# Optimization experiments

Hardware: AMD Instinct MI355X
Metric: run time of the kernel (lower is better)

The kernel has to match this reference:

```python
import jax, jax.numpy as jnp
import numpy as np

B, N, D = 512, 256, 16   # batch, tokens (num_patches+1), embed_dim (= n_qubits)
STAGES = 4               # log2(D) butterfly stages


def _safe_acos(u):
    # matches torch acos + nan_to_num: out-of-range -> 0, with clean gradients
    ok = jnp.abs(u) <= 1.0
    return jnp.where(ok, jnp.arccos(jnp.clip(u, -1.0, 1.0)), 0.0)


def get_rbs_parameters(x):
    # x: [B, N, D] -> RBS angles [B, N, D-1]; recursive spherical-coordinate decomposition
    a0 = _safe_acos(x[..., 0])
    def step(carry, xi):
        t, a_prev = carry
        inv = jnp.nan_to_num(1.0 / jnp.sin(a_prev))
        t = t * inv
        a = _safe_acos(xi * t)
        return (t, a), a
    xs = jnp.moveaxis(x[..., 1:D - 1], -1, 0)  # [D-2, B, N]
    _, rest = jax.lax.scan(step, (jnp.ones_like(a0), a0), xs)
    alphas = jnp.concatenate([a0[None], rest], axis=0)  # [D-1, B, N]
    return jnp.moveaxis(alphas, 0, -1)


def amplitudes(alphas):
    # unary-state amplitudes prepared by the diagonal vector loader
    # a_i = cos(alpha_i) * prod_{k<i} sin(alpha_k);  a_{D-1} = prod_k sin(alpha_k)
    sins = jnp.sin(alphas)
    prefix = jnp.concatenate([jnp.ones_like(sins[..., :1]), jnp.cumprod(sins, axis=-1)], axis=-1)  # [B,N,D]
    return jnp.concatenate([prefix[..., :D - 1] * jnp.cos(alphas), prefix[..., D - 1:]], axis=-1)


def butterfly_matrix(angles):
    # orthogonal DxD matrix implemented by the Butterfly RBS circuit in the unary subspace
    d = 2 * angles.shape[1]
    M = jnp.eye(d, dtype=angles.dtype)
    for s in range(angles.shape[0]):
        step = 1 << s
        idx_i = np.array([i for i in range(d) if (i // step) % 2 == 0])
        idx_j = idx_i + step
        c = jnp.cos(angles[s])[:, None]
        sn = jnp.sin(angles[s])[:, None]
        Mi, Mj = M[idx_i], M[idx_j]
        M = M.at[idx_i].set(c * Mi + sn * Mj)
        M = M.at[idx_j].set(-sn * Mi + c * Mj)
    return M


def layer_norm(x, g, b, eps=1e-5):
    mu = jnp.mean(x, -1, keepdims=True)
    var = jnp.var(x, -1, keepdims=True)
    return (x - mu) / jnp.sqrt(var + eps) * g + b


def setup_inputs() -> dict:
    key = jax.random.key(0)
    ks = jax.random.split(key, 4)
    return {
        "x": jax.random.normal(ks[0], (B, N, D), jnp.float32),
        "ln1_g": jnp.ones((D,), jnp.float32),
        "ln1_b": jnp.zeros((D,), jnp.float32),
        "angles": jax.random.normal(ks[1], (STAGES, D // 2), jnp.float32),
        "ln2_g": jnp.ones((D,), jnp.float32),
        "ln2_b": jnp.zeros((D,), jnp.float32),
        "w1": jax.random.normal(ks[2], (D, 4 * D), jnp.float32) / np.sqrt(D).astype(np.float32),
        "b1": jnp.zeros((4 * D,), jnp.float32),
        "w2": jax.random.normal(ks[3], (4 * D, D), jnp.float32) / np.sqrt(4 * D).astype(np.float32),
        "b2": jnp.zeros((D,), jnp.float32),
    }


def reference(x, ln1_g, ln1_b, angles, ln2_g, ln2_b, w1, b1, w2, b2):
    inp = layer_norm(x, ln1_g, ln1_b) / 2.0
    alphas = jnp.nan_to_num(get_rbs_parameters(inp))
    a = amplitudes(alphas)                 # [B,N,D] loaded unary amplitudes
    W = butterfly_matrix(angles)           # [D,D] orthogonal butterfly
    Wa = jnp.einsum('de,bne->bnd', W, a)   # [B,N,D]
    vxT = jnp.abs(Wa)
    # xwx[b,i,j] = sqrt(P(qubit0=1)) = |<a_j| W |a_i>| for the xWx circuit
    xwx = jnp.abs(jnp.einsum('bid,bjd->bij', Wa, a))
    attn = jax.nn.softmax(xwx, axis=-1)
    x = x + jnp.einsum('bij,bjd->bid', attn, vxT)
    h = layer_norm(x, ln2_g, ln2_b)
    h = jax.nn.gelu(h @ w1 + b1, approximate=False) @ w2 + b2
    return x + h
```

## Files before the change

kernel.cpp:

```cpp
#include <hip/hip_runtime.h>
#include <math.h>

#define NTOK 256
#define DD 16
#define BDIM 256

typedef short short8 __attribute__((ext_vector_type(8)));
typedef float f32x16 __attribute__((ext_vector_type(16)));
typedef unsigned int u32;
typedef unsigned long long u64;

__device__ __forceinline__ u32 f2bf(float f) {
    u32 u = __float_as_uint(f);
    u += 0x7FFFu + ((u >> 16) & 1u);
    return u >> 16;
}
struct U128 { u64 a, b; };
__device__ __forceinline__ short8 ld8(const unsigned short* p) {
    U128 t;
    t.a = *(const u64*)(p);
    t.b = *(const u64*)(p + 4);
    return __builtin_bit_cast(short8, t);
}
__device__ __forceinline__ void pack_swap16(f32x16 p, short8& f0, short8& f1) {
    u32 W00, W01, W10, W11, W20, W21, W30, W31;
    asm("v_cvt_pk_bf16_f32 %0, %1, %2" : "=v"(W00) : "v"(p[0]),  "v"(p[1]));
    asm("v_cvt_pk_bf16_f32 %0, %1, %2" : "=v"(W01) : "v"(p[2]),  "v"(p[3]));
    asm("v_cvt_pk_bf16_f32 %0, %1, %2" : "=v"(W10) : "v"(p[4]),  "v"(p[5]));
    asm("v_cvt_pk_bf16_f32 %0, %1, %2" : "=v"(W11) : "v"(p[6]),  "v"(p[7]));
    asm("v_cvt_pk_bf16_f32 %0, %1, %2" : "=v"(W20) : "v"(p[8]),  "v"(p[9]));
    asm("v_cvt_pk_bf16_f32 %0, %1, %2" : "=v"(W21) : "v"(p[10]), "v"(p[11]));
    asm("v_cvt_pk_bf16_f32 %0, %1, %2" : "=v"(W30) : "v"(p[12]), "v"(p[13]));
    asm("v_cvt_pk_bf16_f32 %0, %1, %2" : "=v"(W31) : "v"(p[14]), "v"(p[15]));
    asm("v_permlane32_swap_b32 %0, %1" : "+v"(W00), "+v"(W10));
    asm("v_permlane32_swap_b32 %0, %1" : "+v"(W01), "+v"(W11));
    asm("v_permlane32_swap_b32 %0, %1" : "+v"(W20), "+v"(W30));
    asm("v_permlane32_swap_b32 %0, %1" : "+v"(W21), "+v"(W31));
    struct { u32 x, y, z, w; } i0{W00, W01, W10, W11}, i1{W20, W21, W30, W31};
    f0 = __builtin_bit_cast(short8, i0);
    f1 = __builtin_bit_cast(short8, i1);
}
__device__ __forceinline__ float gelu_erf(float v) {
    float xx = v * 0.70710678118654752f;
    float ax = fabsf(xx);
    float t = __builtin_amdgcn_rcpf(__builtin_fmaf(0.3275911f, ax, 1.0f));
    float poly = t * (0.254829592f + t * (-0.284496736f + t * (1.421413741f
               + t * (-1.453152027f + t * 1.061405429f))));
    float r = 1.0f - poly * __expf(-ax * ax);
    float e = copysignf(r, xx);
    return 0.5f * v * (1.0f + e);
}

__global__ __launch_bounds__(BDIM, 4) void qab_kernel(
    const float* __restrict__ x,
    const float* __restrict__ ln1_g, const float* __restrict__ ln1_b,
    const float* __restrict__ angles,
    const float* __restrict__ ln2_g, const float* __restrict__ ln2_b,
    const float* __restrict__ w1, const float* __restrict__ b1,
    const float* __restrict__ w2, const float* __restrict__ b2,
    float* __restrict__ out)
{
    __shared__ alignas(16) unsigned short a_bf[NTOK][20];
    __shared__ alignas(16) unsigned short wa_bf[NTOK][20];
    __shared__ alignas(16) unsigned short vxT[17][268];
    __shared__ alignas(16) unsigned short w1tb[64][20];
    __shared__ alignas(16) unsigned short w2tb[16][68];
    __shared__ alignas(16) float b1_lds[64];
    __shared__ alignas(16) float ln2g_lds[DD];
    __shared__ alignas(16) float ln2b_lds[DD];
    __shared__ alignas(16) float b2_lds[DD];

    const int b     = blockIdx.x >> 1;
    const int half  = blockIdx.x & 1;
    const int tid   = threadIdx.x;
    const int r     = tid;
    const int wv    = tid >> 6;
    const int strip = half * 4 + wv;
    const int l31   = tid & 31;
    const int hi    = (tid >> 5) & 1;
    const int lane  = tid & 63;

    const float* xres = x + ((size_t)b * NTOK + 32 * strip + l31) * DD;
    const float4 xra = *(const float4*)(xres + 4 * hi);
    const float4 xrb = *(const float4*)(xres + 8 + 4 * hi);

    f32x16 zc;
    #pragma unroll
    for (int t = 0; t < 16; ++t) zc[t] = 0.0f;

    float amp[DD];
    {
        const float* xrow = x + ((size_t)b * NTOK + r) * DD;
        float xr[DD];
        #pragma unroll
        for (int qq = 0; qq < 4; ++qq) {
            float4 v = ((const float4*)xrow)[qq];
            xr[4*qq+0] = v.x; xr[4*qq+1] = v.y; xr[4*qq+2] = v.z; xr[4*qq+3] = v.w;
        }
        float mu = 0.0f;
        #pragma unroll
        for (int d = 0; d < DD; ++d) mu += xr[d];
        mu *= (1.0f / DD);
        float var = 0.0f;
        #pragma unroll
        for (int d = 0; d < DD; ++d) { float dv = xr[d] - mu; var += dv * dv; }
        var *= (1.0f / DD);
        float rs = 1.0f / sqrtf(var + 1e-5f);
        float inp[DD];
        #pragma unroll
        for (int d = 0; d < DD; ++d)
            inp[d] = ((xr[d] - mu) * rs * ln1_g[d] + ln1_b[d]) * 0.5f;

        float P = 1.0f;
        #pragma unroll
        for (int i = 0; i < DD - 1; ++i) {
            float v = inp[i];
            float v2 = v * v;
            bool ok = v2 <= P;
            amp[i] = ok ? v : __builtin_amdgcn_sqrtf(P);
            P = ok ? __builtin_fmaf(-v, v, P) : 0.0f;
        }
        amp[DD - 1] = __builtin_amdgcn_sqrtf(P);
    }

    {
        u32 aw[8];
        #pragma unroll
        for (int k = 0; k < 8; ++k)
            asm("v_cvt_pk_bf16_f32 %0, %1, %2" : "=v"(aw[k]) : "v"(amp[2*k]), "v"(amp[2*k+1]));
        *(u64*)&a_bf[r][0]  = (u64)aw[0] | ((u64)aw[1] << 32);
        *(u64*)&a_bf[r][4]  = (u64)aw[2] | ((u64)aw[3] << 32);
        *(u64*)&a_bf[r][8]  = (u64)aw[4] | ((u64)aw[5] << 32);
        *(u64*)&a_bf[r][12] = (u64)aw[6] | ((u64)aw[7] << 32);
    }

    {
        float sn_l = 0.0f, cs_l = 0.0f;
        if (lane < 32) __sincosf(angles[lane], &sn_l, &cs_l);
        #pragma unroll
        for (int s = 0; s < 4; ++s) {
            const int step = 1 << s;
            #pragma unroll
            for (int p = 0; p < 8; ++p) {
                const int i = ((p >> s) << (s + 1)) | (p & (step - 1));
                const int j = i + step;
                float sn = __shfl(sn_l, s * 8 + p, 64);
                float cs = __shfl(cs_l, s * 8 + p, 64);
                float vi = amp[i], vj = amp[j];
                amp[i] =  cs * vi + sn * vj;
                amp[j] = -sn * vi + cs * vj;
            }
        }
        u32 ww[8];
        #pragma unroll
        for (int k = 0; k < 8; ++k)
            asm("v_cvt_pk_bf16_f32 %0, %1, %2" : "=v"(ww[k]) : "v"(amp[2*k]), "v"(amp[2*k+1]));
        *(u64*)&wa_bf[r][0]  = (u64)ww[0] | ((u64)ww[1] << 32);
        *(u64*)&wa_bf[r][4]  = (u64)ww[2] | ((u64)ww[3] << 32);
        *(u64*)&wa_bf[r][8]  = (u64)ww[4] | ((u64)ww[5] << 32);
        *(u64*)&wa_bf[r][12] = (u64)ww[6] | ((u64)ww[7] << 32);
        #pragma unroll
        for (int d = 0; d < DD; ++d)
            vxT[d][r] = (unsigned short)f2bf(fabsf(amp[d]));
    }

    for (int i = r; i < 64 * DD; i += BDIM) {
        w1tb[i & 63][i >> 6] = (unsigned short)f2bf(w1[i]);
        w2tb[i & 15][i >> 4] = (unsigned short)f2bf(w2[i]);
    }
    if (r < 64) b1_lds[r] = b1[r];
    else if (r < 80)  ln2g_lds[r - 64] = ln2_g[r - 64];
    else if (r < 96)  ln2b_lds[r - 80] = ln2_b[r - 80];
    else if (r < 112) b2_lds[r - 96]  = b2[r - 96];
    vxT[16][r] = 0x3F80;
    __syncthreads();

    const int ncl = (l31 < 16) ? l31 : 16;
    f32x16 Oacc = zc;
    {
        short8 waf = ld8(&wa_bf[32 * strip + l31][8 * hi]);
        #pragma unroll
        for (int jt = 0; jt < 8; ++jt) {
            short8 af = ld8(&a_bf[jt * 32 + l31][8 * hi]);
            f32x16 S = __builtin_amdgcn_mfma_f32_32x32x16_bf16(af, waf, zc, 0, 0, 0);
            f32x16 pv;
            #pragma unroll
            for (int t = 0; t < 16; ++t) pv[t] = __expf(fabsf(S[t]));
            short8 pb0, pb1;
            pack_swap16(pv, pb0, pb1);
            short8 va0 = ld8(&vxT[ncl][jt * 32 + 8 * hi]);
            short8 va1 = ld8(&vxT[ncl][jt * 32 + 16 + 8 * hi]);
            Oacc = __builtin_amdgcn_mfma_f32_32x32x16_bf16(va0, pb0, Oacc, 0, 0, 0);
            Oacc = __builtin_amdgcn_mfma_f32_32x32x16_bf16(va1, pb1, Oacc, 0, 0, 0);
        }
    }

    const float rl = 1.0f / Oacc[8];
    float o1[8];
    o1[0] = xra.x + Oacc[0] * rl;  o1[1] = xra.y + Oacc[1] * rl;
    o1[2] = xra.z + Oacc[2] * rl;  o1[3] = xra.w + Oacc[3] * rl;
    o1[4] = xrb.x + Oacc[4] * rl;  o1[5] = xrb.y + Oacc[5] * rl;
    o1[6] = xrb.z + Oacc[6] * rl;  o1[7] = xrb.w + Oacc[7] * rl;

    float s8 = 0.0f;
    #pragma unroll
    for (int t = 0; t < 8; ++t) s8 += o1[t];
    float mu2 = (s8 + __shfl_xor(s8, 32, 64)) * (1.0f / DD);
    float v8 = 0.0f;
    #pragma unroll
    for (int t = 0; t < 8; ++t) { float dv = o1[t] - mu2; v8 += dv * dv; }
    float var2 = (v8 + __shfl_xor(v8, 32, 64)) * (1.0f / DD);
    float rs2 = 1.0f / sqrtf(var2 + 1e-5f);

    const float4 g0v = *(const float4*)&ln2g_lds[4 * hi];
    const float4 g1v = *(const float4*)&ln2g_lds[8 + 4 * hi];
    const float4 bb0 = *(const float4*)&ln2b_lds[4 * hi];
    const float4 bb1 = *(const float4*)&ln2b_lds[8 + 4 * hi];
    float h[8];
    h[0] = (o1[0]-mu2)*rs2*g0v.x + bb0.x;  h[1] = (o1[1]-mu2)*rs2*g0v.y + bb0.y;
    h[2] = (o1[2]-mu2)*rs2*g0v.z + bb0.z;  h[3] = (o1[3]-mu2)*rs2*g0v.w + bb0.w;
    h[4] = (o1[4]-mu2)*rs2*g1v.x + bb1.x;  h[5] = (o1[5]-mu2)*rs2*g1v.y + bb1.y;
    h[6] = (o1[6]-mu2)*rs2*g1v.z + bb1.z;  h[7] = (o1[7]-mu2)*rs2*g1v.w + bb1.w;

    short8 hB;
    {
        u32 w0, w1u, w2u, w3;
        asm("v_cvt_pk_bf16_f32 %0, %1, %2" : "=v"(w0)  : "v"(h[0]), "v"(h[1]));
        asm("v_cvt_pk_bf16_f32 %0, %1, %2" : "=v"(w1u) : "v"(h[2]), "v"(h[3]));
        asm("v_cvt_pk_bf16_f32 %0, %1, %2" : "=v"(w2u) : "v"(h[4]), "v"(h[5]));
        asm("v_cvt_pk_bf16_f32 %0, %1, %2" : "=v"(w3)  : "v"(h[6]), "v"(h[7]));
        asm("s_nop 1\n\tv_permlane32_swap_b32 %0, %1" : "+v"(w0),  "+v"(w2u));
        asm("s_nop 1\n\tv_permlane32_swap_b32 %0, %1" : "+v"(w1u), "+v"(w3));
        struct { u32 x, y, z, w; } hw{w0, w1u, w2u, w3};
        hB = __builtin_bit_cast(short8, hw);
    }

    const int dcl = (l31 < 15) ? l31 : 15;
    f32x16 O2 = zc;
    {
        const float4 c0 = *(const float4*)&b2_lds[4 * hi];
        const float4 c1 = *(const float4*)&b2_lds[8 + 4 * hi];
        O2[0] = c0.x; O2[1] = c0.y; O2[2] = c0.z; O2[3] = c0.w;
        O2[4] = c1.x; O2[5] = c1.y; O2[6] = c1.z; O2[7] = c1.w;
    }
    #pragma unroll
    for (int kblk = 0; kblk < 2; ++kblk) {
        f32x16 Hc;
        {
            const float* bp = &b1_lds[32 * kblk];
            const float4 c0 = *(const float4*)(bp + 4 * hi);
            const float4 c1 = *(const float4*)(bp + 8 + 4 * hi);
            const float4 c2 = *(const float4*)(bp + 16 + 4 * hi);
            const float4 c3 = *(const float4*)(bp + 24 + 4 * hi);
            Hc[0]=c0.x; Hc[1]=c0.y; Hc[2]=c0.z; Hc[3]=c0.w;
            Hc[4]=c1.x; Hc[5]=c1.y; Hc[6]=c1.z; Hc[7]=c1.w;
            Hc[8]=c2.x; Hc[9]=c2.y; Hc[10]=c2.z; Hc[11]=c2.w;
            Hc[12]=c3.x; Hc[13]=c3.y; Hc[14]=c3.z; Hc[15]=c3.w;
        }
        short8 w1f = ld8(&w1tb[32 * kblk + l31][8 * hi]);
        f32x16 H = __builtin_amdgcn_mfma_f32_32x32x16_bf16(w1f, hB, Hc, 0, 0, 0);
        f32x16 gv;
        #pragma unroll
        for (int t = 0; t < 16; ++t) gv[t] = gelu_erf(H[t]);
        short8 gb0, gb1;
        pack_swap16(gv, gb0, gb1);
        short8 w2f0 = ld8(&w2tb[dcl][32 * kblk + 8 * hi]);
        short8 w2f1 = ld8(&w2tb[dcl][32 * kblk + 16 + 8 * hi]);
        O2 = __builtin_amdgcn_mfma_f32_32x32x16_bf16(w2f0, gb0, O2, 0, 0, 0);
        O2 = __builtin_amdgcn_mfma_f32_32x32x16_bf16(w2f1, gb1, O2, 0, 0, 0);
    }

    {
        float* orow = out + ((size_t)b * NTOK + 32 * strip + l31) * DD;
        float4 oa, ob;
        oa.x = o1[0] + O2[0]; oa.y = o1[1] + O2[1];
        oa.z = o1[2] + O2[2]; oa.w = o1[3] + O2[3];
        ob.x = o1[4] + O2[4]; ob.y = o1[5] + O2[5];
        ob.z = o1[6] + O2[6]; ob.w = o1[7] + O2[7];
        *(float4*)(orow + 4 * hi) = oa;
        *(float4*)(orow + 8 + 4 * hi) = ob;
    }
}

extern "C" void kernel_launch(void* const* d_in, const int* in_sizes, int n_in,
                              void* d_out, int out_size, void* d_ws, size_t ws_size,
                              hipStream_t stream) {
    const float* x     = (const float*)d_in[0];
    const float* ln1_g = (const float*)d_in[1];
    const float* ln1_b = (const float*)d_in[2];
    const float* ang   = (const float*)d_in[3];
    const float* ln2_g = (const float*)d_in[4];
    const float* ln2_b = (const float*)d_in[5];
    const float* w1    = (const float*)d_in[6];
    const float* b1    = (const float*)d_in[7];
    const float* w2    = (const float*)d_in[8];
    const float* b2    = (const float*)d_in[9];
    float* out = (float*)d_out;

    const int B = in_sizes[0] / (NTOK * DD);
    hipLaunchKernelGGL(qab_kernel, dim3(2 * B), dim3(BDIM), 0, stream,
                       x, ln1_g, ln1_b, ang, ln2_g, ln2_b, w1, b1, w2, b2, out);
}
```

Measured before the change: 21.81 us.

## Double block size and split attention key tiles across wave pairs

Raises the block to 512 threads. The two halves of the block split the prologue: one half writes the bf16 amplitudes and stages the weights, the other runs the butterfly and writes the value transpose. Each attention strip is handled by two waves, each covering half of the key tiles. The partial accumulators are then reduced through LDS that reuses the amplitude buffer, which costs two extra barriers. The intent is to shorten the serial MFMA/exp chain per wave and raise parallelism, at the cost of redundant LN1 work in both halves and a final reduction in which half the waves sit idle.

```diff
diff --git a/kernel.cpp b/kernel.cpp
--- a/kernel.cpp
+++ b/kernel.cpp
@@ -3,7 +3,7 @@
 
 #define NTOK 256
 #define DD 16
-#define BDIM 256
+#define BDIM 512
 
 typedef short short8 __attribute__((ext_vector_type(8)));
 typedef float f32x16 __attribute__((ext_vector_type(16)));
@@ -51,7 +51,7 @@
     return 0.5f * v * (1.0f + e);
 }
 
-__global__ __launch_bounds__(BDIM, 4) void qab_kernel(
+__global__ __launch_bounds__(BDIM, 8) void qab_kernel(
     const float* __restrict__ x,
     const float* __restrict__ ln1_g, const float* __restrict__ ln1_b,
     const float* __restrict__ angles,
@@ -70,12 +70,15 @@
     __shared__ alignas(16) float ln2b_lds[DD];
     __shared__ alignas(16) float b2_lds[DD];
 
-    const int b     = blockIdx.x >> 1;
-    const int half  = blockIdx.x & 1;
+    const int bb    = blockIdx.x;
+    const int b     = bb >> 1;
+    const int half  = bb & 1;
     const int tid   = threadIdx.x;
-    const int r     = tid;
-    const int wv    = tid >> 6;
-    const int strip = half * 4 + wv;
+    const int r     = tid & (NTOK - 1);
+    const int q     = tid >> 8;
+    const int w     = tid >> 6;
+    const int strip = half * 4 + (w >> 1);
+    const int jh    = w & 1;
     const int l31   = tid & 31;
     const int hi    = (tid >> 5) & 1;
     const int lane  = tid & 63;
@@ -123,7 +126,7 @@
         amp[DD - 1] = __builtin_amdgcn_sqrtf(P);
     }
 
-    {
+    if (q == 0) {
         u32 aw[8];
         #pragma unroll
         for (int k = 0; k < 8; ++k)
@@ -132,9 +135,16 @@
         *(u64*)&a_bf[r][4]  = (u64)aw[2] | ((u64)aw[3] << 32);
         *(u64*)&a_bf[r][8]  = (u64)aw[4] | ((u64)aw[5] << 32);
         *(u64*)&a_bf[r][12] = (u64)aw[6] | ((u64)aw[7] << 32);
-    }
-
-    {
+        for (int i = r; i < 64 * DD; i += NTOK) {
+            w1tb[i & 63][i >> 6] = (unsigned short)f2bf(w1[i]);
+            w2tb[i & 15][i >> 4] = (unsigned short)f2bf(w2[i]);
+        }
+        if (r >= 128 && r < 192) b1_lds[r - 128] = b1[r - 128];
+        if (r >= 192 && r < 208) ln2g_lds[r - 192] = ln2_g[r - 192];
+        if (r >= 208 && r < 224) ln2b_lds[r - 208] = ln2_b[r - 208];
+        if (r >= 224 && r < 240) b2_lds[r - 224] = b2[r - 224];
+        vxT[16][r] = 0x3F80;
+    } else {
         float sn_l = 0.0f, cs_l = 0.0f;
         if (lane < 32) __sincosf(angles[lane], &sn_l, &cs_l);
         #pragma unroll
@@ -163,16 +173,6 @@
         for (int d = 0; d < DD; ++d)
             vxT[d][r] = (unsigned short)f2bf(fabsf(amp[d]));
     }
-
-    for (int i = r; i < 64 * DD; i += BDIM) {
-        w1tb[i & 63][i >> 6] = (unsigned short)f2bf(w1[i]);
-        w2tb[i & 15][i >> 4] = (unsigned short)f2bf(w2[i]);
-    }
-    if (r < 64) b1_lds[r] = b1[r];
-    else if (r < 80)  ln2g_lds[r - 64] = ln2_g[r - 64];
-    else if (r < 96)  ln2b_lds[r - 80] = ln2_b[r - 80];
-    else if (r < 112) b2_lds[r - 96]  = b2[r - 96];
-    vxT[16][r] = 0x3F80;
     __syncthreads();
 
     const int ncl = (l31 < 16) ? l31 : 16;
@@ -180,7 +180,8 @@
     {
         short8 waf = ld8(&wa_bf[32 * strip + l31][8 * hi]);
         #pragma unroll
-        for (int jt = 0; jt < 8; ++jt) {
+        for (int jj = 0; jj < 4; ++jj) {
+            const int jt = 4 * jh + jj;
             short8 af = ld8(&a_bf[jt * 32 + l31][8 * hi]);
             f32x16 S = __builtin_amdgcn_mfma_f32_32x32x16_bf16(af, waf, zc, 0, 0, 0);
             f32x16 pv;
@@ -193,6 +194,25 @@
             Oacc = __builtin_amdgcn_mfma_f32_32x32x16_bf16(va0, pb0, Oacc, 0, 0, 0);
             Oacc = __builtin_amdgcn_mfma_f32_32x32x16_bf16(va1, pb1, Oacc, 0, 0, 0);
         }
+    }
+
+    __syncthreads();
+    float* part = (float*)a_bf;
+    if (jh == 1) {
+        float* pr = part + (((w >> 1) * 64) + l31 * 2 + hi) * 10;
+        float2 p0; p0.x = Oacc[0]; p0.y = Oacc[1]; *(float2*)&pr[0] = p0;
+        float2 p1; p1.x = Oacc[2]; p1.y = Oacc[3]; *(float2*)&pr[2] = p1;
+        float2 p2; p2.x = Oacc[4]; p2.y = Oacc[5]; *(float2*)&pr[4] = p2;
+        float2 p3; p3.x = Oacc[6]; p3.y = Oacc[7]; *(float2*)&pr[6] = p3;
+        pr[8] = Oacc[8];
+    }
+    __syncthreads();
+    if (jh == 1) return;
+
+    {
+        const float* pr = part + (((w >> 1) * 64) + l31 * 2 + hi) * 10;
+        #pragma unroll
+        for (int k = 0; k < 9; ++k) Oacc[k] += pr[k];
     }
 
     const float rl = 1.0f / Oacc[8];
```

Result: slower. 25.21 us (+15.6%).
